# Optimization experiments

Measured on AMD Instinct MI355X. Metric: run time of the kernel, lower is better.

The kernel has to match this reference:

```python
import jax, jax.numpy as jnp
import numpy as np

B, IN, OUT = 8192, 4096, 4096

def setup_inputs() -> dict:
    key = jax.random.key(0)
    ks = jax.random.split(key, 7)
    # sigma params initialized near -3 as in the torch module
    return {
        "x": jax.random.normal(ks[0], (B, IN), dtype=jnp.float32),
        "weight_mu": 0.1 * jax.random.normal(ks[1], (OUT, IN), dtype=jnp.float32),
        "weight_sigma": -3.0 + 0.1 * jax.random.normal(ks[2], (OUT, IN), dtype=jnp.float32),
        "bias_mu": 0.1 * jax.random.normal(ks[3], (OUT,), dtype=jnp.float32),
        "bias_sigma": -3.0 + 0.1 * jax.random.normal(ks[4], (OUT,), dtype=jnp.float32),
        "eps_w": jax.random.normal(ks[5], (OUT, IN), dtype=jnp.float32),
        "eps_b": jax.random.normal(ks[6], (OUT,), dtype=jnp.float32),
    }

def reference(x, weight_mu, weight_sigma, bias_mu, bias_sigma, eps_w, eps_b):
    # Reparameterized sample: w = mu + exp(sigma) * eps
    weight = weight_mu + jnp.exp(weight_sigma) * eps_w          # [OUT, IN]
    bias = bias_mu + jnp.exp(bias_sigma) * eps_b                # [OUT]
    out = jnp.einsum('bi,oi->bo', x, weight) + bias             # [B, OUT]
    # KL(q || N(0,1)); note log(var) == 2*sigma
    weight_var = jnp.exp(2.0 * weight_sigma)
    bias_var = jnp.exp(2.0 * bias_sigma)
    kl_w = -0.5 * jnp.sum(1.0 + 2.0 * weight_sigma - weight_mu ** 2 - weight_var)
    kl_b = -0.5 * jnp.sum(1.0 + 2.0 * bias_sigma - bias_mu ** 2 - bias_var)
    return out, kl_w + kl_b
```

## Files before the change

### kernel.cpp

```cpp
#include <hip/hip_runtime.h>

#define MDIM 8192
#define NDIM 4096
#define KDIM 4096

typedef unsigned short u16;
typedef __attribute__((ext_vector_type(8))) short short8;
typedef __attribute__((ext_vector_type(4))) float f32x4;

__device__ __forceinline__ u16 f2b(float f) {
  unsigned u = __float_as_uint(f);
  u += 0x7FFFu + ((u >> 16) & 1u);
  return (u16)(u >> 16);
}
__device__ __forceinline__ unsigned pk2(float a, float b) {
  return (unsigned)f2b(a) | ((unsigned)f2b(b) << 16);
}

__device__ __forceinline__ void async16(const u16* g, u16* l) {
  __builtin_amdgcn_global_load_lds(
      (const __attribute__((address_space(1))) unsigned*)g,
      (__attribute__((address_space(3))) unsigned*)l, 16, 0, 0);
}

__global__ __launch_bounds__(256) void k_prep(const float4* __restrict__ wmu,
                                              const float4* __restrict__ wsg,
                                              const float4* __restrict__ wep,
                                              uint4* __restrict__ wb,
                                              const float4* __restrict__ x,
                                              uint4* __restrict__ xb,
                                              float* __restrict__ partials) {
  const int bx = blockIdx.x;
  if (bx < 8192) {
    const int i = bx * 256 + (int)threadIdx.x;
    float part = 0.f;
    uint4 o;
    {
      float4 m = wmu[2 * i], s = wsg[2 * i], e = wep[2 * i];
      float e0 = __expf(s.x), e1 = __expf(s.y), e2 = __expf(s.z), e3 = __expf(s.w);
      o.x = pk2(m.x + e0 * e.x, m.y + e1 * e.y);
      o.y = pk2(m.z + e2 * e.z, m.w + e3 * e.w);
      part += (1.f + 2.f * s.x - m.x * m.x - e0 * e0)
            + (1.f + 2.f * s.y - m.y * m.y - e1 * e1)
            + (1.f + 2.f * s.z - m.z * m.z - e2 * e2)
            + (1.f + 2.f * s.w - m.w * m.w - e3 * e3);
    }
    {
      float4 m = wmu[2 * i + 1], s = wsg[2 * i + 1], e = wep[2 * i + 1];
      float e0 = __expf(s.x), e1 = __expf(s.y), e2 = __expf(s.z), e3 = __expf(s.w);
      o.z = pk2(m.x + e0 * e.x, m.y + e1 * e.y);
      o.w = pk2(m.z + e2 * e.z, m.w + e3 * e.w);
      part += (1.f + 2.f * s.x - m.x * m.x - e0 * e0)
            + (1.f + 2.f * s.y - m.y * m.y - e1 * e1)
            + (1.f + 2.f * s.z - m.z * m.z - e2 * e2)
            + (1.f + 2.f * s.w - m.w * m.w - e3 * e3);
    }
    wb[i] = o;
    for (int off = 32; off; off >>= 1) part += __shfl_down(part, off, 64);
    __shared__ float red[4];
    const int lane = threadIdx.x & 63, wv = threadIdx.x >> 6;
    if (lane == 0) red[wv] = part;
    __syncthreads();
    if (threadIdx.x == 0)
      partials[bx] = red[0] + red[1] + red[2] + red[3];
  } else {
    const int i0 = (bx - 8192) * 256 + (int)threadIdx.x;
#pragma unroll
    for (int c = 0; c < 2; ++c) {
      const int i = i0 + c * (8192 * 256);
      float4 a = x[2 * i], b = x[2 * i + 1];
      uint4 o;
      o.x = pk2(a.x, a.y); o.y = pk2(a.z, a.w);
      o.z = pk2(b.x, b.y); o.w = pk2(b.z, b.w);
      xb[i] = o;
    }
  }
}

__global__ __launch_bounds__(1024) void k_bias(const float* __restrict__ bmu,
                                               const float* __restrict__ bsg,
                                               const float* __restrict__ bep,
                                               float* __restrict__ bias,
                                               const float* __restrict__ partials,
                                               int nPart,
                                               float* __restrict__ klOut) {
  float part = 0.f;
  for (int i = threadIdx.x; i < NDIM; i += 1024) {
    float s = bsg[i], m = bmu[i];
    float es = __expf(s);
    bias[i] = m + es * bep[i];
    part += 1.f + 2.f * s - m * m - es * es;
  }
  for (int i = threadIdx.x; i < nPart; i += 1024) part += partials[i];
  for (int off = 32; off; off >>= 1) part += __shfl_down(part, off, 64);
  __shared__ float red[16];
  const int lane = threadIdx.x & 63, wv = threadIdx.x >> 6;
  if (lane == 0) red[wv] = part;
  __syncthreads();
  if (threadIdx.x == 0) {
    float s = 0.f;
#pragma unroll
    for (int w = 0; w < 16; ++w) s += red[w];
    *klOut = -0.5f * s;
  }
}

__global__ __launch_bounds__(512, 2) void k_gemm(const u16* __restrict__ A,
                                                 const u16* __restrict__ B,
                                                 const float* __restrict__ bias,
                                                 float* __restrict__ C) {
  __shared__ u16 sA[2][2][8192];
  __shared__ u16 sB[2][2][8192];

  const int tid = threadIdx.x;
  const int wave = tid >> 6, lane = tid & 63;
  const int fr = lane & 15;
  const int fg = lane >> 4;
  const int fgp = fg ^ ((fr >> 1) & 3);
  const int wm128 = (wave >> 2) * 128;
  const int wn64  = (wave & 3) * 64;
  const int w512  = wave << 9;

  const int bm = (blockIdx.x & 31) * 256;
  const int bn = (blockIdx.x >> 5) * 256;

  const int gq = (tid & 3) ^ ((tid >> 3) & 3);
  const u16* gA = A + (size_t)(bm + (tid >> 2)) * KDIM + gq * 8;
  const u16* gB = B + (size_t)(bn + (tid >> 2)) * KDIM + gq * 8;

#define STG(g, larr, ks)                                                     \
  do {                                                                       \
    async16((g) + (ks), &(larr)[0] + w512);                                  \
    async16((g) + (size_t)128 * KDIM + (ks), &(larr)[0] + 4096 + w512);      \
  } while (0)

  f32x4 acc[8][4] = {};
  short8 af[4], bf[4];

  STG(gA, sA[0][0], 0);
  STG(gB, sB[0][0], 0);
  STG(gA, sA[0][1], 32);
  STG(gB, sB[0][1], 32);
  STG(gA, sA[1][0], 64);
  STG(gB, sB[1][0], 64);
  asm volatile("s_waitcnt vmcnt(4)" ::: "memory");
  __builtin_amdgcn_s_barrier();

#define PHASE(BUF, H, QM, RDB, STAGE_STMT, TILE_END)                          \
  {                                                                           \
    _Pragma("unroll") for (int x = 0; x < 4; ++x) {                           \
      af[x] = *(const short8*)&sA[BUF][H][(wm128 + (QM)*64 + x*16 + fr)*32 + fgp*8]; \
      if (RDB)                                                                \
        bf[x] = *(const short8*)&sB[BUF][H][(wn64 + x*16 + fr)*32 + fgp*8];   \
    }                                                                         \
    STAGE_STMT;                                                               \
    __builtin_amdgcn_s_barrier();                                             \
    asm volatile("s_waitcnt lgkmcnt(0)" ::: "memory");                        \
    __builtin_amdgcn_sched_barrier(0);                                        \
    __builtin_amdgcn_s_setprio(1);                                            \
    _Pragma("unroll") for (int x = 0; x < 4; ++x)                             \
      _Pragma("unroll") for (int y = 0; y < 4; ++y)                           \
        acc[(QM)*4 + x][y] = __builtin_amdgcn_mfma_f32_16x16x32_bf16(         \
            af[x], bf[y], acc[(QM)*4 + x][y], 0, 0, 0);                       \
    __builtin_amdgcn_s_setprio(0);                                            \
    if (TILE_END) asm volatile("s_waitcnt vmcnt(4)" ::: "memory");            \
    __builtin_amdgcn_s_barrier();                                             \
  }

  for (int i = 0; i < 32; ++i) {
    const int t = 2 * i;
    int s1 = t + 1; if (s1 > 63) s1 = 63;
    int s2 = t + 2; if (s2 > 63) s2 = 63;
    int s3 = t + 3; if (s3 > 63) s3 = 63;
    const int k1  = s1 * 64 + 32;
    const int k2a = s2 * 64;
    const int k2b = s2 * 64 + 32;
    const int k3  = s3 * 64;

    PHASE(0, 0, 0, 1, STG(gA, sA[1][1], k1),  false)
    PHASE(0, 0, 1, 0, STG(gB, sB[1][1], k1),  false)
    PHASE(0, 1, 0, 1, STG(gA, sA[0][0], k2a), false)
    PHASE(0, 1, 1, 0, STG(gB, sB[0][0], k2a), true)
    PHASE(1, 0, 0, 1, STG(gA, sA[0][1], k2b), false)
    PHASE(1, 0, 1, 0, STG(gB, sB[0][1], k2b), false)
    PHASE(1, 1, 0, 1, STG(gA, sA[1][0], k3),  false)
    PHASE(1, 1, 1, 0, STG(gB, sB[1][0], k3),  true)
  }
#undef PHASE
#undef STG

#pragma unroll
  for (int y = 0; y < 4; ++y) {
    const int gn = bn + wn64 + y * 16 + fr;
    const float bv = bias[gn];
#pragma unroll
    for (int x = 0; x < 8; ++x) {
      const int gm0 = bm + wm128 + x * 16 + fg * 4;
      float* Cp = C + (size_t)gm0 * NDIM + gn;
#pragma unroll
      for (int r = 0; r < 4; ++r)
        Cp[(size_t)r * NDIM] = acc[x][y][r] + bv;
    }
  }
}

extern "C" void kernel_launch(void* const* d_in, const int* in_sizes, int n_in,
                              void* d_out, int out_size, void* d_ws, size_t ws_size,
                              hipStream_t stream) {
  const float* x    = (const float*)d_in[0];
  const float* wmu  = (const float*)d_in[1];
  const float* wsig = (const float*)d_in[2];
  const float* bmu  = (const float*)d_in[3];
  const float* bsig = (const float*)d_in[4];
  const float* ew   = (const float*)d_in[5];
  const float* eb   = (const float*)d_in[6];
  float* out = (float*)d_out;

  char* ws = (char*)d_ws;
  u16*   xb       = (u16*)ws;
  u16*   wb       = (u16*)(ws + 67108864);
  float* bias     = (float*)(ws + 100663296);
  float* partials = (float*)(ws + 100679680);

  k_prep<<<16384, 256, 0, stream>>>((const float4*)wmu, (const float4*)wsig,
                                    (const float4*)ew, (uint4*)wb,
                                    (const float4*)x, (uint4*)xb, partials);
  k_bias<<<1, 1024, 0, stream>>>(bmu, bsig, eb, bias, partials, 8192,
                                 out + (size_t)MDIM * NDIM);
  k_gemm<<<512, 512, 0, stream>>>(xb, wb, bias, out);
}
```

Measured before the change: 617.2 us.

## Double-buffer MFMA operand fragments in registers to overlap LDS reads with MFMAs

Operand fragments are now double-buffered in registers (afA/afB, bfA/bfB). Each phase issues the LDS reads for the next phase's fragments right after the barrier, then waits only on the older reads via a partial lgkmcnt before running its MFMAs. The global-load vmcnt wait moves ahead of the barrier in the tile-ending phases, so the prefetch reads see completed stages. The goal is to hide LDS read latency behind matrix-core work. The cost is extra VGPRs for the second fragment set, which may hurt occupancy, and a more fragile hand-tuned waitcnt schedule.

```diff
diff --git a/kernel.cpp b/kernel.cpp
--- a/kernel.cpp
+++ b/kernel.cpp
@@ -134,8 +134,16 @@
     async16((g) + (size_t)128 * KDIM + (ks), &(larr)[0] + 4096 + w512);      \
   } while (0)
 
+  short8 afA[4], afB[4], bfA[4], bfB[4];
+
+#define LD_AF(DST, BUF, H, QM)                                               \
+  _Pragma("unroll") for (int x = 0; x < 4; ++x)                              \
+    DST[x] = *(const short8*)&sA[BUF][H][(wm128 + (QM)*64 + x*16 + fr)*32 + fgp*8];
+#define LD_BF(DST, BUF, H)                                                   \
+  _Pragma("unroll") for (int x = 0; x < 4; ++x)                              \
+    DST[x] = *(const short8*)&sB[BUF][H][(wn64 + x*16 + fr)*32 + fgp*8];
+
   f32x4 acc[8][4] = {};
-  short8 af[4], bf[4];
 
   STG(gA, sA[0][0], 0);
   STG(gB, sB[0][0], 0);
@@ -145,25 +153,23 @@
   STG(gB, sB[1][0], 64);
   asm volatile("s_waitcnt vmcnt(4)" ::: "memory");
   __builtin_amdgcn_s_barrier();
-
-#define PHASE(BUF, H, QM, RDB, STAGE_STMT, TILE_END)                          \
+  LD_AF(afA, 0, 0, 0);
+  LD_BF(bfA, 0, 0);
+
+#define PHASE(CAF, CBF, QM, STAGE_STMT, VMW, RA_STMT, RA_N)                   \
   {                                                                           \
-    _Pragma("unroll") for (int x = 0; x < 4; ++x) {                           \
-      af[x] = *(const short8*)&sA[BUF][H][(wm128 + (QM)*64 + x*16 + fr)*32 + fgp*8]; \
-      if (RDB)                                                                \
-        bf[x] = *(const short8*)&sB[BUF][H][(wn64 + x*16 + fr)*32 + fgp*8];   \
-    }                                                                         \
     STAGE_STMT;                                                               \
+    if (VMW) asm volatile("s_waitcnt vmcnt(4)" ::: "memory");                 \
     __builtin_amdgcn_s_barrier();                                             \
-    asm volatile("s_waitcnt lgkmcnt(0)" ::: "memory");                        \
+    RA_STMT;                                                                  \
+    asm volatile("s_waitcnt lgkmcnt(" RA_N ")" ::: "memory");                 \
     __builtin_amdgcn_sched_barrier(0);                                        \
     __builtin_amdgcn_s_setprio(1);                                            \
     _Pragma("unroll") for (int x = 0; x < 4; ++x)                             \
       _Pragma("unroll") for (int y = 0; y < 4; ++y)                           \
         acc[(QM)*4 + x][y] = __builtin_amdgcn_mfma_f32_16x16x32_bf16(         \
-            af[x], bf[y], acc[(QM)*4 + x][y], 0, 0, 0);                       \
+            CAF[x], CBF[y], acc[(QM)*4 + x][y], 0, 0, 0);                     \
     __builtin_amdgcn_s_setprio(0);                                            \
-    if (TILE_END) asm volatile("s_waitcnt vmcnt(4)" ::: "memory");            \
     __builtin_amdgcn_s_barrier();                                             \
   }
 
@@ -177,17 +183,19 @@
     const int k2b = s2 * 64 + 32;
     const int k3  = s3 * 64;
 
-    PHASE(0, 0, 0, 1, STG(gA, sA[1][1], k1),  false)
-    PHASE(0, 0, 1, 0, STG(gB, sB[1][1], k1),  false)
-    PHASE(0, 1, 0, 1, STG(gA, sA[0][0], k2a), false)
-    PHASE(0, 1, 1, 0, STG(gB, sB[0][0], k2a), true)
-    PHASE(1, 0, 0, 1, STG(gA, sA[0][1], k2b), false)
-    PHASE(1, 0, 1, 0, STG(gB, sB[0][1], k2b), false)
-    PHASE(1, 1, 0, 1, STG(gA, sA[1][0], k3),  false)
-    PHASE(1, 1, 1, 0, STG(gB, sB[1][0], k3),  true)
+    PHASE(afA, bfA, 0, STG(gA, sA[1][1], k1),  0, LD_AF(afB,0,0,1),                 "4")
+    PHASE(afB, bfA, 1, STG(gB, sB[1][1], k1),  0, LD_AF(afA,0,1,0); LD_BF(bfB,0,1), "8")
+    PHASE(afA, bfB, 0, STG(gA, sA[0][0], k2a), 0, LD_AF(afB,0,1,1),                 "4")
+    PHASE(afB, bfB, 1, STG(gB, sB[0][0], k2a), 1, LD_AF(afA,1,0,0); LD_BF(bfA,1,0), "8")
+    PHASE(afA, bfA, 0, STG(gA, sA[0][1], k2b), 0, LD_AF(afB,1,0,1),                 "4")
+    PHASE(afB, bfA, 1, STG(gB, sB[0][1], k2b), 0, LD_AF(afA,1,1,0); LD_BF(bfB,1,1), "8")
+    PHASE(afA, bfB, 0, STG(gA, sA[1][0], k3),  0, LD_AF(afB,1,1,1),                 "4")
+    PHASE(afB, bfB, 1, STG(gB, sB[1][0], k3),  1, LD_AF(afA,0,0,0); LD_BF(bfA,0,0), "8")
   }
 #undef PHASE
 #undef STG
+#undef LD_AF
+#undef LD_BF
 
 #pragma unroll
   for (int y = 0; y < 4; ++y) {
```

New measurement: 640.1 us. 3.7% more time.
